# Optimization experiments

Measured on AMD Instinct MI355X. Metric: run time of the kernel, lower is better.

The kernel has to match this reference:

```python
import jax, jax.numpy as jnp
import numpy as np

S, H, I, E, TOP_K = 8192, 2048, 2048, 8, 2


def setup_inputs() -> dict:
    key = jax.random.key(0)
    k0, k1, k2, k3 = jax.random.split(key, 4)
    scale = 1.0 / np.sqrt(H)
    return {
        "hidden_states": jax.random.normal(k0, (S, H), dtype=jnp.float32),
        "w_gate": jax.random.normal(k1, (E, H), dtype=jnp.float32) * scale,
        "w1": jax.random.normal(k2, (E, 2 * I, H), dtype=jnp.float32) * scale,
        "w2": jax.random.normal(k3, (E, H, I), dtype=jnp.float32) * (1.0 / np.sqrt(I)),
        "top_k": TOP_K,
    }


def reference(hidden_states, w_gate, w1, w2, top_k):
    # Router: logits -> float32 softmax -> top-k -> renormalize
    router_logits = hidden_states @ w_gate.T                      # [S, E]
    probs = jax.nn.softmax(router_logits.astype(jnp.float32), axis=-1)
    top_p, top_i = jax.lax.top_k(probs, top_k)                    # [S, k]
    top_p = top_p / jnp.sum(top_p, axis=-1, keepdims=True)

    n_tok, n_exp = probs.shape
    # Dense combine weights [S, E]; zero for non-selected experts.
    combine = jnp.zeros((n_tok, n_exp), dtype=probs.dtype)
    combine = combine.at[jnp.arange(n_tok)[:, None], top_i].add(top_p)

    inter = w2.shape[2]
    out = jnp.zeros_like(hidden_states)
    # Loop over the small fixed expert set; masked-combine gives exact
    # fused_moe semantics (scatter-combine of weighted expert outputs).
    for e in range(n_exp):
        gu = hidden_states @ w1[e].T                              # [S, 2I]
        gate, up = gu[:, :inter], gu[:, inter:]
        h = jax.nn.silu(gate) * up                                # SiluAndMul
        out = out + combine[:, e:e + 1].astype(hidden_states.dtype) * (h @ w2[e].T)
    return out, router_logits
```

## Files before the change

### kernel.cpp

```cpp
#include <hip/hip_runtime.h>
#include <hip/hip_bf16.h>
#include <stdint.h>

#define S_TOK 8192
#define H_DIM 2048
#define I_DIM 2048
#define E_NUM 8

typedef __attribute__((ext_vector_type(4))) float f32x4;
typedef __attribute__((ext_vector_type(8))) short bf16x8;
typedef __attribute__((ext_vector_type(8))) unsigned short u16x8;

#define MFMA16(a, b, c) __builtin_amdgcn_mfma_f32_16x16x32_bf16((a), (b), (c), 0, 0, 0)

__device__ __forceinline__ unsigned short f2bf(float f) {
    unsigned int u = __float_as_uint(f);
    unsigned int r = (u + 0x7FFFu + ((u >> 16) & 1u)) >> 16;
    return (unsigned short)r;
}
__device__ __forceinline__ float bf2f(unsigned short u) {
    return __uint_as_float((unsigned int)u << 16);
}

__device__ __forceinline__ void cvt8(const float* __restrict__ s, unsigned short* __restrict__ d) {
    float4 v0 = *(const float4*)s;
    float4 v1 = *(const float4*)(s + 4);
    u16x8 o;
    o[0] = f2bf(v0.x); o[1] = f2bf(v0.y); o[2] = f2bf(v0.z); o[3] = f2bf(v0.w);
    o[4] = f2bf(v1.x); o[5] = f2bf(v1.y); o[6] = f2bf(v1.z); o[7] = f2bf(v1.w);
    *(u16x8*)d = o;
}

__device__ __forceinline__ void async_copy16(void* lds, const void* g) {
    __builtin_amdgcn_global_load_lds(
        (const __attribute__((address_space(1))) void*)(uintptr_t)g,
        (__attribute__((address_space(3))) void*)(uintptr_t)lds,
        16, 0, 0);
}

__device__ __forceinline__ int xcd_swizzle(int bid, int nwg) {
    int cpx = nwg >> 3;
    return (bid & 7) * cpx + (bid >> 3);
}

__global__ void cvt_kernel(const float* __restrict__ src, unsigned short* __restrict__ dst, long n) {
    long i0 = ((long)blockIdx.x * blockDim.x + threadIdx.x) * 8;
    long stride = (long)gridDim.x * blockDim.x * 8;
    for (long i = i0; i < n; i += stride) cvt8(src + i, dst + i);
}

template<int HALF>
__device__ __forceinline__ void cvt_w1_half_body(const float* __restrict__ src,
                                                 unsigned short* __restrict__ dst,
                                                 long i0, long stride) {
    const long CH = 1L << 21;
    const long TOT = (long)E_NUM * 2 * CH;
    for (long j = i0; j < TOT; j += stride) {
        long e = j >> 22;
        long piece = (j >> 21) & 1;
        long off = j & (CH - 1);
        long g = (e << 23) + ((piece * 2 + HALF) << 21) + off;
        cvt8(src + g, dst + g);
    }
}

template<int HALF>
__global__ void cvt_w1_half_kernel(const float* __restrict__ src, unsigned short* __restrict__ dst) {
    long i0 = ((long)blockIdx.x * blockDim.x + threadIdx.x) * 8;
    long stride = (long)gridDim.x * blockDim.x * 8;
    cvt_w1_half_body<HALF>(src, dst, i0, stride);
}

__global__ void router_kernel(const float* __restrict__ hs, const float* __restrict__ wg,
                              float* __restrict__ logits,
                              unsigned int* __restrict__ tchoice, float* __restrict__ twgt,
                              unsigned short* __restrict__ hsb) {
    int t = blockIdx.x;
    int tid = threadIdx.x;
    const float* hrow = hs + (size_t)t * H_DIM;
    float4 h0 = *(const float4*)(hrow + tid * 8);
    float4 h1 = *(const float4*)(hrow + tid * 8 + 4);
    u16x8 o;
    o[0] = f2bf(h0.x); o[1] = f2bf(h0.y); o[2] = f2bf(h0.z); o[3] = f2bf(h0.w);
    o[4] = f2bf(h1.x); o[5] = f2bf(h1.y); o[6] = f2bf(h1.z); o[7] = f2bf(h1.w);
    *(u16x8*)(hsb + (size_t)t * H_DIM + tid * 8) = o;

    float p[E_NUM];
#pragma unroll
    for (int e = 0; e < E_NUM; ++e) {
        const float* w = wg + (size_t)e * H_DIM + tid * 8;
        float4 w0 = *(const float4*)(w);
        float4 w1v = *(const float4*)(w + 4);
        p[e] = h0.x * w0.x + h0.y * w0.y + h0.z * w0.z + h0.w * w0.w +
               h1.x * w1v.x + h1.y * w1v.y + h1.z * w1v.z + h1.w * w1v.w;
    }
#pragma unroll
    for (int e = 0; e < E_NUM; ++e)
#pragma unroll
        for (int d = 32; d > 0; d >>= 1) p[e] += __shfl_xor(p[e], d, 64);

    __shared__ float red[4][E_NUM];
    int wave = tid >> 6, lane = tid & 63;
    if (lane == 0) {
#pragma unroll
        for (int e = 0; e < E_NUM; ++e) red[wave][e] = p[e];
    }
    __syncthreads();
    if (tid == 0) {
        float l[E_NUM];
#pragma unroll
        for (int e = 0; e < E_NUM; ++e) l[e] = red[0][e] + red[1][e] + red[2][e] + red[3][e];
#pragma unroll
        for (int e = 0; e < E_NUM; ++e) logits[(size_t)t * E_NUM + e] = l[e];
        int i1 = 0;
#pragma unroll
        for (int e = 1; e < E_NUM; ++e) if (l[e] > l[i1]) i1 = e;
        int i2 = (i1 == 0) ? 1 : 0;
#pragma unroll
        for (int e = 0; e < E_NUM; ++e) if (e != i1 && l[e] > l[i2]) i2 = e;
        float b = __expf(l[i2] - l[i1]);
        tchoice[t] = (unsigned)i1 | ((unsigned)i2 << 4);
        twgt[t] = 1.0f / (1.0f + b);
    }
}

__global__ __launch_bounds__(1024) void scan_kernel(
    const unsigned int* __restrict__ tchoice, const float* __restrict__ twgt,
    int* __restrict__ cnt, int* __restrict__ off,
    int* __restrict__ tok_of, float* __restrict__ wgt_of,
    unsigned int* __restrict__ slot_of) {
    __shared__ int lcnt[E_NUM][1024];
    __shared__ int tot[E_NUM];
    int tid = threadIdx.x;
    unsigned int ch[8];
    int c[E_NUM];
#pragma unroll
    for (int e = 0; e < E_NUM; ++e) c[e] = 0;
#pragma unroll
    for (int k = 0; k < 8; ++k) {
        ch[k] = tchoice[tid * 8 + k];
        c[ch[k] & 15]++;
        c[(ch[k] >> 4) & 15]++;
    }
#pragma unroll
    for (int e = 0; e < E_NUM; ++e) lcnt[e][tid] = c[e];
    __syncthreads();
    int wave = tid >> 6, lane = tid & 63;
    if (wave < E_NUM) {
        int base = 0;
        for (int chk = 0; chk < 16; ++chk) {
            int v = lcnt[wave][chk * 64 + lane];
            int inc = v;
#pragma unroll
            for (int d = 1; d < 64; d <<= 1) {
                int u = __shfl_up(inc, d, 64);
                if (lane >= d) inc += u;
            }
            lcnt[wave][chk * 64 + lane] = base + inc - v;
            base += __shfl(inc, 63, 64);
        }
        if (lane == 0) tot[wave] = base;
    }
    __syncthreads();
    if (tid == 0) {
        int s = 0;
#pragma unroll
        for (int e = 0; e < E_NUM; ++e) { off[e] = s; cnt[e] = tot[e]; s += tot[e]; }
    }
    __syncthreads();
#pragma unroll
    for (int e = 0; e < E_NUM; ++e) c[e] = lcnt[e][tid];
#pragma unroll
    for (int k = 0; k < 8; ++k) {
        int t = tid * 8 + k;
        int i1 = ch[k] & 15, i2 = (ch[k] >> 4) & 15;
        float wA = twgt[t];
        int s1 = c[i1]++;
        int s2 = c[i2]++;
        tok_of[i1 * S_TOK + s1] = t; wgt_of[i1 * S_TOK + s1] = wA;
        tok_of[i2 * S_TOK + s2] = t; wgt_of[i2 * S_TOK + s2] = 1.0f - wA;
        slot_of[2 * t]     = ((unsigned)i1 << 20) | (unsigned)s1;
        slot_of[2 * t + 1] = ((unsigned)i2 << 20) | (unsigned)s2;
    }
}

__global__ void combine_kernel(const unsigned short* __restrict__ pbuf,
                               const unsigned int* __restrict__ slot_of,
                               const int* __restrict__ off, float* __restrict__ out) {
    int t = blockIdx.x, tid = threadIdx.x;
    unsigned int a = slot_of[2 * t], b = slot_of[2 * t + 1];
    size_t ra = (size_t)(off[a >> 20] + (int)(a & 0xFFFFFu));
    size_t rb = (size_t)(off[b >> 20] + (int)(b & 0xFFFFFu));
    const unsigned short* pa = pbuf + ra * H_DIM + tid * 8;
    const unsigned short* pb = pbuf + rb * H_DIM + tid * 8;
    ushort4 a0 = *(const ushort4*)pa, a1 = *(const ushort4*)(pa + 4);
    ushort4 b0 = *(const ushort4*)pb, b1 = *(const ushort4*)(pb + 4);
    float4 r0, r1;
    r0.x = bf2f(a0.x) + bf2f(b0.x); r0.y = bf2f(a0.y) + bf2f(b0.y);
    r0.z = bf2f(a0.z) + bf2f(b0.z); r0.w = bf2f(a0.w) + bf2f(b0.w);
    r1.x = bf2f(a1.x) + bf2f(b1.x); r1.y = bf2f(a1.y) + bf2f(b1.y);
    r1.z = bf2f(a1.z) + bf2f(b1.z); r1.w = bf2f(a1.w) + bf2f(b1.w);
    float* op = out + (size_t)t * H_DIM + tid * 8;
    *(float4*)op = r0;
    *(float4*)(op + 4) = r1;
}

template<int IS_G1>
__global__ __launch_bounds__(512, 2) void moe_gemm_kernel(
    const unsigned short* __restrict__ A_src, const unsigned short* __restrict__ W,
    const int* __restrict__ cnt, const int* __restrict__ off,
    const int* __restrict__ tok_of, const float* __restrict__ wgt_of,
    unsigned short* __restrict__ dst,
    const float* __restrict__ cvt_src, unsigned short* __restrict__ cvt_dst,
    long cvt_n, int gemm_grid, int cvt_blks, int nt_base, int cvt_mode) {
    if ((int)blockIdx.x >= gemm_grid) {
        long i0 = ((long)((int)blockIdx.x - gemm_grid) * blockDim.x + threadIdx.x) * 8;
        long stride = (long)cvt_blks * blockDim.x * 8;
        if (cvt_mode == 2) {
            cvt_w1_half_body<1>(cvt_src, cvt_dst, i0, stride);
        } else {
            for (long i = i0; i < cvt_n; i += stride) cvt8(cvt_src + i, cvt_dst + i);
        }
        return;
    }
    int bx = xcd_swizzle(blockIdx.x, gemm_grid);
    int nt = nt_base + bx / (E_NUM * 32);
    int rr = bx % (E_NUM * 32);
    int e = rr / 32;
    int mt = rr % 32;
    int C = cnt[e];
    if (mt * 256 >= C) return;
    int O = off[e];

    __shared__ __align__(16) char ldsA[2][32768];
    __shared__ __align__(16) char ldsB[2][32768];

    int tid = threadIdx.x;
    int wave = tid >> 6, lane = tid & 63;
    int wr = wave >> 2, wc = wave & 3;

    const char* aptr[4];
#pragma unroll
    for (int q = 0; q < 4; ++q) {
        int row = q * 64 + wave * 8 + (lane >> 3);
        int cu = (lane & 7) ^ (row & 7);
        int grow = mt * 256 + row; if (grow > C - 1) grow = C - 1;
        size_t arow = IS_G1 ? (size_t)tok_of[e * S_TOK + grow] : (size_t)(O + grow);
        aptr[q] = (const char*)(A_src + arow * 2048 + cu * 8);
    }
    const char* bptr[4];
#pragma unroll
    for (int j = 0; j < 4; ++j) {
        int lrow = j * 64 + wave * 8 + (lane >> 3);
        int cu = (lane & 7) ^ (lrow & 7);
        int np = lrow >> 7, wcg = (lrow >> 5) & 3, rem = lrow & 31;
        int tbrow = wcg * 64 + np * 32 + rem;
        size_t brow;
        if (IS_G1) {
            int jj = tbrow & 63, wq = tbrow >> 6;
            if (jj < 32) brow = (size_t)(nt * 128 + wq * 32 + jj);
            else         brow = (size_t)I_DIM + nt * 128 + wq * 32 + (jj - 32);
            brow += (size_t)e * (2 * I_DIM);
        } else {
            brow = (size_t)e * H_DIM + nt * 256 + tbrow;
        }
        bptr[j] = (const char*)(W + brow * 2048 + cu * 8);
    }

    int aoff[8][2], boff[4][2];
#pragma unroll
    for (int m = 0; m < 8; ++m)
#pragma unroll
        for (int ks = 0; ks < 2; ++ks) {
            int row = wr * 128 + m * 16 + (lane & 15);
            int cu = ks * 4 + (lane >> 4);
            aoff[m][ks] = row * 128 + ((cu ^ (row & 7)) * 16);
        }
#pragma unroll
    for (int n = 0; n < 4; ++n)
#pragma unroll
        for (int ks = 0; ks < 2; ++ks) {
            int lrow = (n >> 1) * 128 + wc * 32 + (n & 1) * 16 + (lane & 15);
            int cu = ks * 4 + (lane >> 4);
            boff[n][ks] = lrow * 128 + ((cu ^ (lrow & 7)) * 16);
        }

    f32x4 acc[8][4];
#pragma unroll
    for (int m = 0; m < 8; ++m)
#pragma unroll
        for (int n = 0; n < 4; ++n)
#pragma unroll
            for (int q = 0; q < 4; ++q) acc[m][n][q] = 0.0f;

    auto gA = [&](int q, int T, int buf) {
        async_copy16(ldsA[buf] + q * 8192 + wave * 1024, aptr[q] + T * 128);
    };
    auto gB = [&](int j, int T, int buf) {
        async_copy16(ldsB[buf] + j * 8192 + wave * 1024, bptr[j] + T * 128);
    };

    gA(0, 0, 0); gA(2, 0, 0); gA(1, 0, 0); gA(3, 0, 0);
    gB(0, 0, 0); gB(1, 0, 0);
    gA(0, 1, 1); gA(2, 1, 1); gA(1, 1, 1); gA(3, 1, 1);
    gB(2, 0, 0); gB(3, 0, 0);
    asm volatile("s_waitcnt vmcnt(6)" ::: "memory");
    __builtin_amdgcn_s_barrier();

    bf16x8 ar[8][2], br[2][2];
    int cur = 0;
#pragma unroll 2
    for (int T = 0; T < 32; ++T) {
        int nxt = cur ^ 1;
        int TA = (T + 2 < 32) ? T + 2 : 31;
        int TB = (T + 1 < 32) ? T + 1 : 31;
#pragma unroll
        for (int n = 0; n < 2; ++n)
#pragma unroll
            for (int ks = 0; ks < 2; ++ks)
                br[n][ks] = *(const bf16x8*)(ldsB[cur] + boff[n][ks]);
#pragma unroll
        for (int m = 0; m < 4; ++m)
#pragma unroll
            for (int ks = 0; ks < 2; ++ks)
                ar[m][ks] = *(const bf16x8*)(ldsA[cur] + aoff[m][ks]);
        gB(0, TB, nxt); gB(1, TB, nxt);
        __builtin_amdgcn_s_setprio(1);
#pragma unroll
        for (int m = 0; m < 4; ++m)
#pragma unroll
            for (int n = 0; n < 2; ++n) {
                acc[m][n] = MFMA16(ar[m][0], br[n][0], acc[m][n]);
                acc[m][n] = MFMA16(ar[m][1], br[n][1], acc[m][n]);
            }
        __builtin_amdgcn_s_setprio(0);
        __builtin_amdgcn_s_barrier();
#pragma unroll
        for (int m = 4; m < 8; ++m)
#pragma unroll
            for (int ks = 0; ks < 2; ++ks)
                ar[m][ks] = *(const bf16x8*)(ldsA[cur] + aoff[m][ks]);
        gA(0, TA, cur); gA(2, TA, cur);
        __builtin_amdgcn_s_setprio(1);
#pragma unroll
        for (int m = 4; m < 8; ++m)
#pragma unroll
            for (int n = 0; n < 2; ++n) {
                acc[m][n] = MFMA16(ar[m][0], br[n][0], acc[m][n]);
                acc[m][n] = MFMA16(ar[m][1], br[n][1], acc[m][n]);
            }
        __builtin_amdgcn_s_setprio(0);
        asm volatile("s_waitcnt vmcnt(4)" ::: "memory");
        __builtin_amdgcn_s_barrier();
#pragma unroll
        for (int n = 0; n < 2; ++n)
#pragma unroll
            for (int ks = 0; ks < 2; ++ks)
                br[n][ks] = *(const bf16x8*)(ldsB[cur] + boff[n + 2][ks]);
        gA(1, TA, cur); gA(3, TA, cur);
        __builtin_amdgcn_s_setprio(1);
#pragma unroll
        for (int m = 0; m < 4; ++m)
#pragma unroll
            for (int n = 0; n < 2; ++n) {
                acc[m][n + 2] = MFMA16(ar[m][0], br[n][0], acc[m][n + 2]);
                acc[m][n + 2] = MFMA16(ar[m][1], br[n][1], acc[m][n + 2]);
            }
        __builtin_amdgcn_s_setprio(0);
        __builtin_amdgcn_s_barrier();
        gB(2, TB, nxt); gB(3, TB, nxt);
        __builtin_amdgcn_s_setprio(1);
#pragma unroll
        for (int m = 4; m < 8; ++m)
#pragma unroll
            for (int n = 0; n < 2; ++n) {
                acc[m][n + 2] = MFMA16(ar[m][0], br[n][0], acc[m][n + 2]);
                acc[m][n + 2] = MFMA16(ar[m][1], br[n][1], acc[m][n + 2]);
            }
        __builtin_amdgcn_s_setprio(0);
        asm volatile("s_waitcnt vmcnt(6)" ::: "memory");
        __builtin_amdgcn_s_barrier();
        cur = nxt;
    }

    if (IS_G1) {
#pragma unroll
        for (int m = 0; m < 8; ++m)
#pragma unroll
            for (int q = 0; q < 4; ++q) {
                int row = mt * 256 + wr * 128 + m * 16 + (lane >> 4) * 4 + q;
                if (row < C) {
                    float wgt = wgt_of[e * S_TOK + row];
                    unsigned short* hp = dst + (size_t)(O + row) * I_DIM +
                                         nt * 128 + wc * 32 + (lane & 15);
#pragma unroll
                    for (int n = 0; n < 2; ++n) {
                        float g = acc[m][n][q];
                        float u = acc[m][n + 2][q];
                        float hv = (g / (1.0f + __expf(-g))) * u * wgt;
                        hp[n * 16] = f2bf(hv);
                    }
                }
            }
    } else {
#pragma unroll
        for (int m = 0; m < 8; ++m)
#pragma unroll
            for (int q = 0; q < 4; ++q) {
                int row = mt * 256 + wr * 128 + m * 16 + (lane >> 4) * 4 + q;
                if (row < C) {
                    unsigned short* pp = dst + (size_t)(O + row) * H_DIM +
                                         nt * 256 + wc * 64 + (lane & 15);
#pragma unroll
                    for (int n = 0; n < 4; ++n)
                        pp[n * 16] = f2bf(acc[m][n][q]);
                }
            }
    }
}

extern "C" void kernel_launch(void* const* d_in, const int* in_sizes, int n_in,
                              void* d_out, int out_size, void* d_ws, size_t ws_size,
                              hipStream_t stream) {
    const float* hs = (const float*)d_in[0];
    const float* wg = (const float*)d_in[1];
    const float* w1 = (const float*)d_in[2];
    const float* w2 = (const float*)d_in[3];

    float* out = (float*)d_out;
    float* logits = out + (size_t)S_TOK * H_DIM;

    char* ws = (char*)d_ws;
    int* cnt = (int*)ws;
    int* off = (int*)(ws + 256);
    int* tok_of = (int*)(ws + 512);
    float* wgt_of = (float*)(ws + 512 + (size_t)E_NUM * S_TOK * 4);
    unsigned int* slot_of = (unsigned int*)(ws + 512 + (size_t)E_NUM * S_TOK * 8);
    unsigned int* tchoice = (unsigned int*)(ws + 512 + (size_t)E_NUM * S_TOK * 8 + (size_t)S_TOK * 8);
    float* twgt = (float*)(ws + 512 + (size_t)E_NUM * S_TOK * 8 + (size_t)S_TOK * 12);
    size_t o = 512 + (size_t)E_NUM * S_TOK * 8 + (size_t)S_TOK * 16;
    o = (o + 4095) & ~(size_t)4095;
    unsigned short* hsb = (unsigned short*)(ws + o);  o += (size_t)S_TOK * H_DIM * 2;
    unsigned short* wxb = (unsigned short*)(ws + o);  o += (size_t)E_NUM * 2 * I_DIM * H_DIM * 2;
    unsigned short* hbuf = (unsigned short*)(ws + o); o += (size_t)S_TOK * 2 * I_DIM * 2;
    size_t o_w2 = o;
    size_t need_fused = o_w2 + (size_t)E_NUM * H_DIM * I_DIM * 2;
    bool fused = (ws_size >= need_fused);

    const long W1_N = (long)E_NUM * 2 * I_DIM * H_DIM;
    const long W2_N = (long)E_NUM * H_DIM * I_DIM;
    const int G1H_GRID = E_NUM * 32 * 8;
    const int G2_GRID = E_NUM * 32 * 8;
    const int CVT_BLKS = 1024;

    router_kernel<<<S_TOK, 256, 0, stream>>>(hs, wg, logits, tchoice, twgt, hsb);
    scan_kernel<<<1, 1024, 0, stream>>>(tchoice, twgt, cnt, off, tok_of, wgt_of, slot_of);

    if (fused) {
        unsigned short* w2b = (unsigned short*)(ws + o_w2);
        unsigned short* pbuf = wxb;
        cvt_w1_half_kernel<0><<<4096, 256, 0, stream>>>(w1, wxb);
        moe_gemm_kernel<1><<<G1H_GRID + CVT_BLKS, 512, 0, stream>>>(
            hsb, wxb, cnt, off, tok_of, wgt_of, hbuf,
            w1, wxb, 0, G1H_GRID, CVT_BLKS, 0, 2);
        moe_gemm_kernel<1><<<G1H_GRID + CVT_BLKS, 512, 0, stream>>>(
            hsb, wxb, cnt, off, tok_of, wgt_of, hbuf,
            w2, w2b, W2_N, G1H_GRID, CVT_BLKS, 8, 1);
        moe_gemm_kernel<0><<<G2_GRID, 512, 0, stream>>>(
            hbuf, w2b, cnt, off, tok_of, wgt_of, pbuf,
            nullptr, nullptr, 0, G2_GRID, 0, 0, 0);
        combine_kernel<<<S_TOK, 256, 0, stream>>>(pbuf, slot_of, off, out);
    } else {
        unsigned short* w2b = wxb;
        unsigned short* pbuf = wxb + (size_t)E_NUM * H_DIM * I_DIM;
        cvt_kernel<<<4096, 256, 0, stream>>>(w1, wxb, W1_N);
        moe_gemm_kernel<1><<<E_NUM * 32 * 16, 512, 0, stream>>>(
            hsb, wxb, cnt, off, tok_of, wgt_of, hbuf,
            nullptr, nullptr, 0, E_NUM * 32 * 16, 0, 0, 0);
        cvt_kernel<<<4096, 256, 0, stream>>>(w2, w2b, W2_N);
        moe_gemm_kernel<0><<<G2_GRID, 512, 0, stream>>>(
            hbuf, w2b, cnt, off, tok_of, wgt_of, pbuf,
            nullptr, nullptr, 0, G2_GRID, 0, 0, 0);
        combine_kernel<<<S_TOK, 256, 0, stream>>>(pbuf, slot_of, off, out);
    }
}
```

Before: 607.3 us.

## Load GEMM B operand directly into registers and fuse W1 half conversion into router

The GEMM kernel stops staging the weight (B) tile through LDS: each lane now loads its bf16 B fragments straight from global memory into registers, halving LDS use, and the main loop is simplified to one barrier phase with all MFMAs issued per k-step. Separately, the first-half W1 fp32->bf16 conversion is folded into the router launch as extra blocks, removing one kernel launch and letting conversion overlap routing. The direct global B loads are less coalesced and have no LDS reuse across waves, so global/L2 traffic and latency exposure may rise, while the reduced LDS footprint could raise occupancy.

```diff
diff --git a/kernel.cpp b/kernel.cpp
--- a/kernel.cpp
+++ b/kernel.cpp
@@ -64,17 +64,18 @@
     }
 }
 
-template<int HALF>
-__global__ void cvt_w1_half_kernel(const float* __restrict__ src, unsigned short* __restrict__ dst) {
-    long i0 = ((long)blockIdx.x * blockDim.x + threadIdx.x) * 8;
-    long stride = (long)gridDim.x * blockDim.x * 8;
-    cvt_w1_half_body<HALF>(src, dst, i0, stride);
-}
-
 __global__ void router_kernel(const float* __restrict__ hs, const float* __restrict__ wg,
                               float* __restrict__ logits,
                               unsigned int* __restrict__ tchoice, float* __restrict__ twgt,
-                              unsigned short* __restrict__ hsb) {
+                              unsigned short* __restrict__ hsb,
+                              const float* __restrict__ w1src, unsigned short* __restrict__ w1dst,
+                              int cvt_blks) {
+    if ((int)blockIdx.x >= S_TOK) {
+        long i0 = ((long)((int)blockIdx.x - S_TOK) * blockDim.x + threadIdx.x) * 8;
+        long stride = (long)cvt_blks * blockDim.x * 8;
+        cvt_w1_half_body<0>(w1src, w1dst, i0, stride);
+        return;
+    }
     int t = blockIdx.x;
     int tid = threadIdx.x;
     const float* hrow = hs + (size_t)t * H_DIM;
@@ -233,7 +234,6 @@
     int O = off[e];
 
     __shared__ __align__(16) char ldsA[2][32768];
-    __shared__ __align__(16) char ldsB[2][32768];
 
     int tid = threadIdx.x;
     int wave = tid >> 6, lane = tid & 63;
@@ -248,26 +248,27 @@
         size_t arow = IS_G1 ? (size_t)tok_of[e * S_TOK + grow] : (size_t)(O + grow);
         aptr[q] = (const char*)(A_src + arow * 2048 + cu * 8);
     }
-    const char* bptr[4];
-#pragma unroll
-    for (int j = 0; j < 4; ++j) {
-        int lrow = j * 64 + wave * 8 + (lane >> 3);
-        int cu = (lane & 7) ^ (lrow & 7);
-        int np = lrow >> 7, wcg = (lrow >> 5) & 3, rem = lrow & 31;
-        int tbrow = wcg * 64 + np * 32 + rem;
-        size_t brow;
-        if (IS_G1) {
-            int jj = tbrow & 63, wq = tbrow >> 6;
-            if (jj < 32) brow = (size_t)(nt * 128 + wq * 32 + jj);
-            else         brow = (size_t)I_DIM + nt * 128 + wq * 32 + (jj - 32);
-            brow += (size_t)e * (2 * I_DIM);
-        } else {
-            brow = (size_t)e * H_DIM + nt * 256 + tbrow;
-        }
-        bptr[j] = (const char*)(W + brow * 2048 + cu * 8);
-    }
-
-    int aoff[8][2], boff[4][2];
+
+    const unsigned short* bp[4][2];
+    {
+        int r16 = lane & 15, t4 = lane >> 4;
+#pragma unroll
+        for (int n = 0; n < 4; ++n)
+#pragma unroll
+            for (int ks = 0; ks < 2; ++ks) {
+                size_t brow;
+                if (IS_G1) {
+                    brow = (size_t)e * (2 * I_DIM) + ((n >> 1) ? I_DIM : 0) +
+                           (size_t)(nt * 128 + wc * 32 + (n & 1) * 16 + r16);
+                } else {
+                    brow = (size_t)e * H_DIM +
+                           (size_t)(nt * 256 + wc * 64 + (n >> 1) * 32 + (n & 1) * 16 + r16);
+                }
+                bp[n][ks] = W + brow * 2048 + ks * 32 + t4 * 8;
+            }
+    }
+
+    int aoff[8][2];
 #pragma unroll
     for (int m = 0; m < 8; ++m)
 #pragma unroll
@@ -276,14 +277,6 @@
             int cu = ks * 4 + (lane >> 4);
             aoff[m][ks] = row * 128 + ((cu ^ (row & 7)) * 16);
         }
-#pragma unroll
-    for (int n = 0; n < 4; ++n)
-#pragma unroll
-        for (int ks = 0; ks < 2; ++ks) {
-            int lrow = (n >> 1) * 128 + wc * 32 + (n & 1) * 16 + (lane & 15);
-            int cu = ks * 4 + (lane >> 4);
-            boff[n][ks] = lrow * 128 + ((cu ^ (lrow & 7)) * 16);
-        }
 
     f32x4 acc[8][4];
 #pragma unroll
@@ -296,91 +289,41 @@
     auto gA = [&](int q, int T, int buf) {
         async_copy16(ldsA[buf] + q * 8192 + wave * 1024, aptr[q] + T * 128);
     };
-    auto gB = [&](int j, int T, int buf) {
-        async_copy16(ldsB[buf] + j * 8192 + wave * 1024, bptr[j] + T * 128);
-    };
-
-    gA(0, 0, 0); gA(2, 0, 0); gA(1, 0, 0); gA(3, 0, 0);
-    gB(0, 0, 0); gB(1, 0, 0);
-    gA(0, 1, 1); gA(2, 1, 1); gA(1, 1, 1); gA(3, 1, 1);
-    gB(2, 0, 0); gB(3, 0, 0);
-    asm volatile("s_waitcnt vmcnt(6)" ::: "memory");
+
+    gA(0, 0, 0); gA(1, 0, 0); gA(2, 0, 0); gA(3, 0, 0);
+    gA(0, 1, 1); gA(1, 1, 1); gA(2, 1, 1); gA(3, 1, 1);
+    asm volatile("s_waitcnt vmcnt(4)" ::: "memory");
     __builtin_amdgcn_s_barrier();
 
-    bf16x8 ar[8][2], br[2][2];
+    bf16x8 ar[8][2], brg[4][2];
     int cur = 0;
-#pragma unroll 2
     for (int T = 0; T < 32; ++T) {
-        int nxt = cur ^ 1;
         int TA = (T + 2 < 32) ? T + 2 : 31;
-        int TB = (T + 1 < 32) ? T + 1 : 31;
-#pragma unroll
-        for (int n = 0; n < 2; ++n)
+#pragma unroll
+        for (int n = 0; n < 4; ++n)
 #pragma unroll
             for (int ks = 0; ks < 2; ++ks)
-                br[n][ks] = *(const bf16x8*)(ldsB[cur] + boff[n][ks]);
-#pragma unroll
-        for (int m = 0; m < 4; ++m)
+                brg[n][ks] = *(const bf16x8*)(bp[n][ks] + T * 64);
+#pragma unroll
+        for (int m = 0; m < 8; ++m)
 #pragma unroll
             for (int ks = 0; ks < 2; ++ks)
                 ar[m][ks] = *(const bf16x8*)(ldsA[cur] + aoff[m][ks]);
-        gB(0, TB, nxt); gB(1, TB, nxt);
+        asm volatile("s_waitcnt lgkmcnt(0) vmcnt(8)" ::: "memory");
+        __builtin_amdgcn_s_barrier();
+#pragma unroll
+        for (int q = 0; q < 4; ++q) gA(q, TA, cur);
+        asm volatile("s_waitcnt vmcnt(4)" ::: "memory");
         __builtin_amdgcn_s_setprio(1);
 #pragma unroll
-        for (int m = 0; m < 4; ++m)
-#pragma unroll
-            for (int n = 0; n < 2; ++n) {
-                acc[m][n] = MFMA16(ar[m][0], br[n][0], acc[m][n]);
-                acc[m][n] = MFMA16(ar[m][1], br[n][1], acc[m][n]);
-            }
+        for (int ks = 0; ks < 2; ++ks)
+#pragma unroll
+            for (int m = 0; m < 8; ++m)
+#pragma unroll
+                for (int n = 0; n < 4; ++n)
+                    acc[m][n] = MFMA16(ar[m][ks], brg[n][ks], acc[m][n]);
         __builtin_amdgcn_s_setprio(0);
-        __builtin_amdgcn_s_barrier();
-#pragma unroll
-        for (int m = 4; m < 8; ++m)
-#pragma unroll
-            for (int ks = 0; ks < 2; ++ks)
-                ar[m][ks] = *(const bf16x8*)(ldsA[cur] + aoff[m][ks]);
-        gA(0, TA, cur); gA(2, TA, cur);
-        __builtin_amdgcn_s_setprio(1);
-#pragma unroll
-        for (int m = 4; m < 8; ++m)
-#pragma unroll
-            for (int n = 0; n < 2; ++n) {
-                acc[m][n] = MFMA16(ar[m][0], br[n][0], acc[m][n]);
-                acc[m][n] = MFMA16(ar[m][1], br[n][1], acc[m][n]);
-            }
-        __builtin_amdgcn_s_setprio(0);
-        asm volatile("s_waitcnt vmcnt(4)" ::: "memory");
-        __builtin_amdgcn_s_barrier();
-#pragma unroll
-        for (int n = 0; n < 2; ++n)
-#pragma unroll
-            for (int ks = 0; ks < 2; ++ks)
-                br[n][ks] = *(const bf16x8*)(ldsB[cur] + boff[n + 2][ks]);
-        gA(1, TA, cur); gA(3, TA, cur);
-        __builtin_amdgcn_s_setprio(1);
-#pragma unroll
-        for (int m = 0; m < 4; ++m)
-#pragma unroll
-            for (int n = 0; n < 2; ++n) {
-                acc[m][n + 2] = MFMA16(ar[m][0], br[n][0], acc[m][n + 2]);
-                acc[m][n + 2] = MFMA16(ar[m][1], br[n][1], acc[m][n + 2]);
-            }
-        __builtin_amdgcn_s_setprio(0);
-        __builtin_amdgcn_s_barrier();
-        gB(2, TB, nxt); gB(3, TB, nxt);
-        __builtin_amdgcn_s_setprio(1);
-#pragma unroll
-        for (int m = 4; m < 8; ++m)
-#pragma unroll
-            for (int n = 0; n < 2; ++n) {
-                acc[m][n + 2] = MFMA16(ar[m][0], br[n][0], acc[m][n + 2]);
-                acc[m][n + 2] = MFMA16(ar[m][1], br[n][1], acc[m][n + 2]);
-            }
-        __builtin_amdgcn_s_setprio(0);
-        asm volatile("s_waitcnt vmcnt(6)" ::: "memory");
-        __builtin_amdgcn_s_barrier();
-        cur = nxt;
+        cur ^= 1;
     }
 
     if (IS_G1) {
@@ -453,13 +396,12 @@
     const int G2_GRID = E_NUM * 32 * 8;
     const int CVT_BLKS = 1024;
 
-    router_kernel<<<S_TOK, 256, 0, stream>>>(hs, wg, logits, tchoice, twgt, hsb);
-    scan_kernel<<<1, 1024, 0, stream>>>(tchoice, twgt, cnt, off, tok_of, wgt_of, slot_of);
-
     if (fused) {
         unsigned short* w2b = (unsigned short*)(ws + o_w2);
         unsigned short* pbuf = wxb;
-        cvt_w1_half_kernel<0><<<4096, 256, 0, stream>>>(w1, wxb);
+        router_kernel<<<S_TOK + CVT_BLKS, 256, 0, stream>>>(
+            hs, wg, logits, tchoice, twgt, hsb, w1, wxb, CVT_BLKS);
+        scan_kernel<<<1, 1024, 0, stream>>>(tchoice, twgt, cnt, off, tok_of, wgt_of, slot_of);
         moe_gemm_kernel<1><<<G1H_GRID + CVT_BLKS, 512, 0, stream>>>(
             hsb, wxb, cnt, off, tok_of, wgt_of, hbuf,
             w1, wxb, 0, G1H_GRID, CVT_BLKS, 0, 2);
@@ -473,6 +415,9 @@
     } else {
         unsigned short* w2b = wxb;
         unsigned short* pbuf = wxb + (size_t)E_NUM * H_DIM * I_DIM;
+        router_kernel<<<S_TOK, 256, 0, stream>>>(
+            hs, wg, logits, tchoice, twgt, hsb, nullptr, nullptr, 1);
+        scan_kernel<<<1, 1024, 0, stream>>>(tchoice, twgt, cnt, off, tok_of, wgt_of, slot_of);
         cvt_kernel<<<4096, 256, 0, stream>>>(w1, wxb, W1_N);
         moe_gemm_kernel<1><<<E_NUM * 32 * 16, 512, 0, stream>>>(
             hsb, wxb, cnt, off, tok_of, wgt_of, hbuf,
```

New measurement: 991.1 us. +63.2%, slower.

## Overlap weight conversion with router and reuse idle GEMM tiles for conversion

Applied to the files above, without the earlier changes.

The first half of the w1 fp32-to-bf16 conversion moves from its own kernel into extra blocks appended to the router launch, so it runs alongside routing. In the GEMM kernels the separate conversion blocks are removed. Tiles that have no tokens for their expert (mt beyond the live tile count) instead take a share of the remaining w1/w2 conversion, ranked by a prefix count over experts. This removes a launch and the extra grid blocks, but conversion throughput now depends on how many tiles happen to be empty. If few tiles are empty, the few that are will do a large amount of serial conversion.

```diff
diff --git a/kernel.cpp b/kernel.cpp
--- a/kernel.cpp
+++ b/kernel.cpp
@@ -64,17 +64,18 @@
     }
 }
 
-template<int HALF>
-__global__ void cvt_w1_half_kernel(const float* __restrict__ src, unsigned short* __restrict__ dst) {
-    long i0 = ((long)blockIdx.x * blockDim.x + threadIdx.x) * 8;
-    long stride = (long)gridDim.x * blockDim.x * 8;
-    cvt_w1_half_body<HALF>(src, dst, i0, stride);
-}
-
 __global__ void router_kernel(const float* __restrict__ hs, const float* __restrict__ wg,
                               float* __restrict__ logits,
                               unsigned int* __restrict__ tchoice, float* __restrict__ twgt,
-                              unsigned short* __restrict__ hsb) {
+                              unsigned short* __restrict__ hsb,
+                              const float* __restrict__ w1src, unsigned short* __restrict__ w1dst,
+                              int cvt_blks) {
+    if ((int)blockIdx.x >= S_TOK) {
+        long i0 = ((long)((int)blockIdx.x - S_TOK) * blockDim.x + threadIdx.x) * 8;
+        long stride = (long)cvt_blks * blockDim.x * 8;
+        cvt_w1_half_body<0>(w1src, w1dst, i0, stride);
+        return;
+    }
     int t = blockIdx.x;
     int tid = threadIdx.x;
     const float* hrow = hs + (size_t)t * H_DIM;
@@ -212,10 +213,30 @@
     const int* __restrict__ tok_of, const float* __restrict__ wgt_of,
     unsigned short* __restrict__ dst,
     const float* __restrict__ cvt_src, unsigned short* __restrict__ cvt_dst,
-    long cvt_n, int gemm_grid, int cvt_blks, int nt_base, int cvt_mode) {
-    if ((int)blockIdx.x >= gemm_grid) {
-        long i0 = ((long)((int)blockIdx.x - gemm_grid) * blockDim.x + threadIdx.x) * 8;
-        long stride = (long)cvt_blks * blockDim.x * 8;
+    long cvt_n, int nt_base, int cvt_mode) {
+    const int GRID = E_NUM * 32 * 8;
+    int bx = xcd_swizzle(blockIdx.x, GRID);
+    int nt_rel = bx / (E_NUM * 32);
+    int rr = bx % (E_NUM * 32);
+    int e = rr / 32;
+    int mt = rr % 32;
+    int nt = nt_base + nt_rel;
+    int C = cnt[e];
+    int live = (C + 255) >> 8;
+    int tid = threadIdx.x;
+
+    if (mt >= live) {
+        if (cvt_mode == 0) return;
+        int S = 0, pre = 0;
+#pragma unroll
+        for (int ee = 0; ee < E_NUM; ++ee) {
+            int nulls = 32 - ((cnt[ee] + 255) >> 8);
+            if (ee < e) pre += nulls;
+            S += nulls;
+        }
+        long nrank = (long)nt_rel * S + pre + (mt - live);
+        long i0 = (nrank * 512 + tid) * 8;
+        long stride = (long)8 * S * 512 * 8;
         if (cvt_mode == 2) {
             cvt_w1_half_body<1>(cvt_src, cvt_dst, i0, stride);
         } else {
@@ -223,19 +244,11 @@
         }
         return;
     }
-    int bx = xcd_swizzle(blockIdx.x, gemm_grid);
-    int nt = nt_base + bx / (E_NUM * 32);
-    int rr = bx % (E_NUM * 32);
-    int e = rr / 32;
-    int mt = rr % 32;
-    int C = cnt[e];
-    if (mt * 256 >= C) return;
     int O = off[e];
 
     __shared__ __align__(16) char ldsA[2][32768];
     __shared__ __align__(16) char ldsB[2][32768];
 
-    int tid = threadIdx.x;
     int wave = tid >> 6, lane = tid & 63;
     int wr = wave >> 2, wc = wave & 3;
 
@@ -449,38 +462,36 @@
 
     const long W1_N = (long)E_NUM * 2 * I_DIM * H_DIM;
     const long W2_N = (long)E_NUM * H_DIM * I_DIM;
-    const int G1H_GRID = E_NUM * 32 * 8;
-    const int G2_GRID = E_NUM * 32 * 8;
+    const int GRID = E_NUM * 32 * 8;
     const int CVT_BLKS = 1024;
-
-    router_kernel<<<S_TOK, 256, 0, stream>>>(hs, wg, logits, tchoice, twgt, hsb);
-    scan_kernel<<<1, 1024, 0, stream>>>(tchoice, twgt, cnt, off, tok_of, wgt_of, slot_of);
 
     if (fused) {
         unsigned short* w2b = (unsigned short*)(ws + o_w2);
         unsigned short* pbuf = wxb;
-        cvt_w1_half_kernel<0><<<4096, 256, 0, stream>>>(w1, wxb);
-        moe_gemm_kernel<1><<<G1H_GRID + CVT_BLKS, 512, 0, stream>>>(
-            hsb, wxb, cnt, off, tok_of, wgt_of, hbuf,
-            w1, wxb, 0, G1H_GRID, CVT_BLKS, 0, 2);
-        moe_gemm_kernel<1><<<G1H_GRID + CVT_BLKS, 512, 0, stream>>>(
-            hsb, wxb, cnt, off, tok_of, wgt_of, hbuf,
-            w2, w2b, W2_N, G1H_GRID, CVT_BLKS, 8, 1);
-        moe_gemm_kernel<0><<<G2_GRID, 512, 0, stream>>>(
-            hbuf, w2b, cnt, off, tok_of, wgt_of, pbuf,
-            nullptr, nullptr, 0, G2_GRID, 0, 0, 0);
+        router_kernel<<<S_TOK + CVT_BLKS, 256, 0, stream>>>(
+            hs, wg, logits, tchoice, twgt, hsb, w1, wxb, CVT_BLKS);
+        scan_kernel<<<1, 1024, 0, stream>>>(tchoice, twgt, cnt, off, tok_of, wgt_of, slot_of);
+        moe_gemm_kernel<1><<<GRID, 512, 0, stream>>>(
+            hsb, wxb, cnt, off, tok_of, wgt_of, hbuf, w1, wxb, 0, 0, 2);
+        moe_gemm_kernel<1><<<GRID, 512, 0, stream>>>(
+            hsb, wxb, cnt, off, tok_of, wgt_of, hbuf, w2, w2b, W2_N, 8, 1);
+        moe_gemm_kernel<0><<<GRID, 512, 0, stream>>>(
+            hbuf, w2b, cnt, off, tok_of, wgt_of, pbuf, nullptr, nullptr, 0, 0, 0);
         combine_kernel<<<S_TOK, 256, 0, stream>>>(pbuf, slot_of, off, out);
     } else {
         unsigned short* w2b = wxb;
         unsigned short* pbuf = wxb + (size_t)E_NUM * H_DIM * I_DIM;
+        router_kernel<<<S_TOK, 256, 0, stream>>>(
+            hs, wg, logits, tchoice, twgt, hsb, nullptr, nullptr, 1);
+        scan_kernel<<<1, 1024, 0, stream>>>(tchoice, twgt, cnt, off, tok_of, wgt_of, slot_of);
         cvt_kernel<<<4096, 256, 0, stream>>>(w1, wxb, W1_N);
-        moe_gemm_kernel<1><<<E_NUM * 32 * 16, 512, 0, stream>>>(
-            hsb, wxb, cnt, off, tok_of, wgt_of, hbuf,
-            nullptr, nullptr, 0, E_NUM * 32 * 16, 0, 0, 0);
+        moe_gemm_kernel<1><<<GRID, 512, 0, stream>>>(
+            hsb, wxb, cnt, off, tok_of, wgt_of, hbuf, nullptr, nullptr, 0, 0, 0);
+        moe_gemm_kernel<1><<<GRID, 512, 0, stream>>>(
+            hsb, wxb, cnt, off, tok_of, wgt_of, hbuf, nullptr, nullptr, 0, 8, 0);
         cvt_kernel<<<4096, 256, 0, stream>>>(w2, w2b, W2_N);
-        moe_gemm_kernel<0><<<G2_GRID, 512, 0, stream>>>(
-            hbuf, w2b, cnt, off, tok_of, wgt_of, pbuf,
-            nullptr, nullptr, 0, G2_GRID, 0, 0, 0);
+        moe_gemm_kernel<0><<<GRID, 512, 0, stream>>>(
+            hbuf, w2b, cnt, off, tok_of, wgt_of, pbuf, nullptr, nullptr, 0, 0, 0);
         combine_kernel<<<S_TOK, 256, 0, stream>>>(pbuf, slot_of, off, out);
     }
 }
```

Result: slower. 622.6 us (+2.5%).
